# Performance work log

Measured on AMD Instinct MI355X. Metric: run time of the kernel, lower is better.

The kernel has to match this reference:

```python
import jax, jax.numpy as jnp
import numpy as np

EPS = 0.001  # additive floor applied after relu, as in the torch code


def setup_inputs() -> dict:
    key = jax.random.key(0)
    kA, kB, kW = jax.random.split(key, 3)
    M, N, C, H, W = 512, 64, 128, 8, 8
    A = jax.random.normal(kA, (M, C, H, W), dtype=jnp.float32)
    B = jax.random.normal(kB, (N, C, H, W), dtype=jnp.float32)
    Wg = jax.random.normal(kW, (C, C), dtype=jnp.float32) * 0.01  # Wg.data.normal_(0.0, 0.01)
    return {"A": A, "B": B, "Wg": Wg}


def reference(A, B, Wg):
    # Faithful vectorization of MIMOcom.get_source_dst_max(A, B, dir=True).
    # Torch loops i,j over HxW: B0 = B[:, i, j, :]; G = B0 @ Wg;
    # combination[m, n, p] = sum_c A[m, p, c] * G[n, c]; running max over (i, j).
    M, C, H, W = A.shape
    N = B.shape[0]
    P = H * W
    Af = jnp.transpose(A, (0, 2, 3, 1)).reshape(M, P, C)  # [M, P, C]
    Bf = jnp.transpose(B, (0, 2, 3, 1)).reshape(N, P, C)  # [N, Q, C]
    G = Bf @ Wg                                           # [N, Q, D]
    scores = jnp.einsum('mpd,nqd->mnpq', Af, G)           # [M, N, P, Q]
    comb_max = scores.max(axis=-1)                        # max over B positions q
    return jax.nn.relu(comb_max) + EPS                    # [M, N, P]
```

## Files before the change

### kernel.cpp

```cpp
#include <hip/hip_runtime.h>
#include <hip/hip_bf16.h>
#include <stdint.h>

typedef __attribute__((ext_vector_type(8))) short bf16x8;
typedef __attribute__((ext_vector_type(4))) float f32x4;
typedef __attribute__((ext_vector_type(16))) float f32x16;
using bf16 = __hip_bfloat16;

static constexpr int Mdim = 512;
static constexpr int Ndim = 64;
static constexpr int Cdim = 128;
static constexpr int Pdim = 64;
static constexpr float EPS_ADD = 0.001f;

#define SB0 __builtin_amdgcn_sched_barrier(0)
#define WAITV(N) asm volatile("s_waitcnt vmcnt(" #N ")" ::: "memory")

__device__ __forceinline__ void gll16(const void* gsrc, void* ldst) {
    const __attribute__((address_space(1))) unsigned int* g =
        (const __attribute__((address_space(1))) unsigned int*)gsrc;
    __attribute__((address_space(3))) unsigned int* l =
        (__attribute__((address_space(3))) unsigned int*)(uintptr_t)ldst;
    __builtin_amdgcn_global_load_lds(g, l, 16, 0, 0);
}

__global__ void prep_kernel(const float* __restrict__ A, const float* __restrict__ B,
                            const float* __restrict__ Wg,
                            bf16* __restrict__ Abf, bf16* __restrict__ Gbf) {
    __shared__ float lds[128 * 65];
    const int t = threadIdx.x;

    if (blockIdx.x < 512) {
        const int m = blockIdx.x;
        const float* __restrict__ Am = A + (size_t)m * (Cdim * Pdim);
#pragma unroll
        for (int i = 0; i < 8; ++i) {
            int v = t + i * 256;
            int gidx = v * 4;
            int c = gidx >> 6, p = gidx & 63;
            float4 val = *reinterpret_cast<const float4*>(Am + gidx);
            float* dst = &lds[c * 65 + p];
            dst[0] = val.x; dst[1] = val.y; dst[2] = val.z; dst[3] = val.w;
        }
        __syncthreads();

        bf16* __restrict__ dstm = Abf + (size_t)m * (Pdim * Cdim);
#pragma unroll
        for (int i = 0; i < 16; ++i) {
            int pr = t + i * 256;
            int p = pr >> 6;
            int c = (pr & 63) << 1;
            float f0 = lds[c * 65 + p];
            float f1 = lds[(c + 1) * 65 + p];
            union { bf16 h[2]; unsigned u; } pk;
            pk.h[0] = __float2bfloat16(f0);
            pk.h[1] = __float2bfloat16(f1);
            *reinterpret_cast<unsigned*>(dstm + p * Cdim + c) = pk.u;
        }
    } else {
        const int nb = blockIdx.x - 512;
        const int n  = nb >> 2;
        const int q0 = (nb & 3) * 16;
        const float* __restrict__ Bn = B + (size_t)n * (Cdim * Pdim);
#pragma unroll
        for (int i = 0; i < 8; ++i) {
            int v = t + i * 256;
            int gidx = v * 4;
            int c = gidx >> 6, q = gidx & 63;
            float4 val = *reinterpret_cast<const float4*>(Bn + gidx);
            float* dst = &lds[c * 65 + q];
            dst[0] = val.x; dst[1] = val.y; dst[2] = val.z; dst[3] = val.w;
        }
        __syncthreads();

        const int d  = t & 127;
        const int qb = q0 + (t >> 7) * 8;
        float acc[8] = {0.f, 0.f, 0.f, 0.f, 0.f, 0.f, 0.f, 0.f};
        for (int c = 0; c < 128; ++c) {
            float w = Wg[c * 128 + d];
#pragma unroll
            for (int qi = 0; qi < 8; ++qi)
                acc[qi] = fmaf(lds[c * 65 + qb + qi], w, acc[qi]);
        }
#pragma unroll
        for (int qi = 0; qi < 8; ++qi)
            Gbf[(size_t)(n * 64 + qb + qi) * Cdim + d] = __float2bfloat16(acc[qi]);
    }
}

__global__ __launch_bounds__(256, 2)
void gemm_max_kernel(const bf16* __restrict__ Abf, const bf16* __restrict__ Gbf,
                     float* __restrict__ out) {
    __shared__ bf16 sA[2][64 * 128];
    const int tid  = threadIdx.x;
    const int lane = tid & 63;
    const int w    = tid >> 6;
    const int nw = w >> 1, h = w & 1;
    const int l31 = lane & 31, hi = lane >> 5;
    const int mg = blockIdx.x & 31;
    const int bn = blockIdx.x >> 5;
    const int n  = bn * 2 + nw;

    const char* Abase = (const char*)Abf + (size_t)mg * 16 * 16384;
    auto stageA = [&](int s) {
        char* dst = (char*)&sA[s & 1][0];
        const char* src = Abase + (size_t)s * 16384;
#pragma unroll
        for (int i = 0; i < 4; ++i) {
            int f = (i * 256 + tid) * 16;
            int row = f >> 8;
            int inner = (f & 255) ^ ((row & 7) << 4);
            gll16(src + row * 256 + inner, dst + f);
        }
    };
    stageA(0);

    bf16x8 gf[2][8];
    {
        const bf16* Gp = Gbf + ((size_t)n * 64 + l31) * 128 + hi * 8;
#pragma unroll
        for (int qt = 0; qt < 2; ++qt)
#pragma unroll
            for (int ks = 0; ks < 8; ++ks)
                gf[qt][ks] = *reinterpret_cast<const bf16x8*>(Gp + qt * 32 * 128 + ks * 16);
    }

    f32x16 acc[2];
    const f32x16 z16 = {0.f,0.f,0.f,0.f,0.f,0.f,0.f,0.f,0.f,0.f,0.f,0.f,0.f,0.f,0.f,0.f};

    auto compute = [&](int s) {
        const char* ab = (const char*)&sA[s & 1][0] + (h * 32 + l31) * 256;
#pragma unroll
        for (int ks = 0; ks < 8; ++ks) {
            const int off = (ks * 32 + hi * 16) ^ ((l31 & 7) << 4);
            bf16x8 a = *reinterpret_cast<const bf16x8*>(ab + off);
            acc[0] = __builtin_amdgcn_mfma_f32_32x32x16_bf16(
                gf[0][ks], a, ks == 0 ? z16 : acc[0], 0, 0, 0);
            acc[1] = __builtin_amdgcn_mfma_f32_32x32x16_bf16(
                gf[1][ks], a, ks == 0 ? z16 : acc[1], 0, 0, 0);
        }
    };

    auto epilogue = [&](int s) {
        float v = acc[0][0];
#pragma unroll
        for (int j = 1; j < 16; ++j) v = fmaxf(v, acc[0][j]);
#pragma unroll
        for (int j = 0; j < 16; ++j) v = fmaxf(v, acc[1][j]);
        v = fmaxf(v, __shfl_xor(v, 32));
        if (hi == 0)
            out[(size_t)(mg * 16 + s) * 4096 + n * 64 + h * 32 + l31] =
                fmaxf(v, 0.f) + EPS_ADD;
    };

    WAITV(16); __builtin_amdgcn_s_barrier(); SB0;
    compute(0); SB0; stageA(1); epilogue(0); SB0;

    for (int s = 1; s <= 14; ++s) {
        WAITV(1); __builtin_amdgcn_s_barrier(); SB0;
        compute(s); SB0; stageA(s + 1); epilogue(s); SB0;
    }

    WAITV(1); __builtin_amdgcn_s_barrier(); SB0;
    compute(15); epilogue(15);
}

extern "C" void kernel_launch(void* const* d_in, const int* in_sizes, int n_in,
                              void* d_out, int out_size, void* d_ws, size_t ws_size,
                              hipStream_t stream) {
    const float* A  = (const float*)d_in[0];
    const float* B  = (const float*)d_in[1];
    const float* Wg = (const float*)d_in[2];
    float* out = (float*)d_out;

    bf16* Abf = (bf16*)d_ws;
    bf16* Gbf = (bf16*)((char*)d_ws + (size_t)Mdim * Pdim * Cdim * sizeof(bf16));

    prep_kernel<<<768, 256, 0, stream>>>(A, B, Wg, Abf, Gbf);
    gemm_max_kernel<<<1024, 256, 0, stream>>>(Abf, Gbf, out);
}
```

Baseline: 52.80 us.

## Pre-swizzle A and G into MFMA fragment layout and load A directly to registers

```diff
diff --git a/kernel.cpp b/kernel.cpp
--- a/kernel.cpp
+++ b/kernel.cpp
@@ -3,7 +3,6 @@
 #include <stdint.h>
 
 typedef __attribute__((ext_vector_type(8))) short bf16x8;
-typedef __attribute__((ext_vector_type(4))) float f32x4;
 typedef __attribute__((ext_vector_type(16))) float f32x16;
 using bf16 = __hip_bfloat16;
 
@@ -14,19 +13,10 @@
 static constexpr float EPS_ADD = 0.001f;
 
 #define SB0 __builtin_amdgcn_sched_barrier(0)
-#define WAITV(N) asm volatile("s_waitcnt vmcnt(" #N ")" ::: "memory")
-
-__device__ __forceinline__ void gll16(const void* gsrc, void* ldst) {
-    const __attribute__((address_space(1))) unsigned int* g =
-        (const __attribute__((address_space(1))) unsigned int*)gsrc;
-    __attribute__((address_space(3))) unsigned int* l =
-        (__attribute__((address_space(3))) unsigned int*)(uintptr_t)ldst;
-    __builtin_amdgcn_global_load_lds(g, l, 16, 0, 0);
-}
 
 __global__ void prep_kernel(const float* __restrict__ A, const float* __restrict__ B,
                             const float* __restrict__ Wg,
-                            bf16* __restrict__ Abf, bf16* __restrict__ Gbf) {
+                            bf16* __restrict__ Afrag, bf16* __restrict__ Gfrag) {
     __shared__ float lds[128 * 65];
     const int t = threadIdx.x;
 
@@ -44,7 +34,7 @@
         }
         __syncthreads();
 
-        bf16* __restrict__ dstm = Abf + (size_t)m * (Pdim * Cdim);
+        unsigned* __restrict__ dst32 = (unsigned*)(Afrag + (size_t)m * 8192);
 #pragma unroll
         for (int i = 0; i < 16; ++i) {
             int pr = t + i * 256;
@@ -52,10 +42,12 @@
             int c = (pr & 63) << 1;
             float f0 = lds[c * 65 + p];
             float f1 = lds[(c + 1) * 65 + p];
-            union { bf16 h[2]; unsigned u; } pk;
-            pk.h[0] = __float2bfloat16(f0);
-            pk.h[1] = __float2bfloat16(f1);
-            *reinterpret_cast<unsigned*>(dstm + p * Cdim + c) = pk.u;
+            union { bf16 hh[2]; unsigned u; } pk;
+            pk.hh[0] = __float2bfloat16(f0);
+            pk.hh[1] = __float2bfloat16(f1);
+            int h = p >> 5, l31 = p & 31;
+            int ks = c >> 4, hi = (c >> 3) & 1, e = c & 7;
+            dst32[h * 2048 + ks * 256 + hi * 128 + l31 * 4 + (e >> 1)] = pk.u;
         }
     } else {
         const int nb = blockIdx.x - 512;
@@ -82,16 +74,20 @@
             for (int qi = 0; qi < 8; ++qi)
                 acc[qi] = fmaf(lds[c * 65 + qb + qi], w, acc[qi]);
         }
+        bf16* __restrict__ gdst = Gfrag + (size_t)n * 8192;
+        const int ks = d >> 4, hi = (d >> 3) & 1, e = d & 7;
 #pragma unroll
-        for (int qi = 0; qi < 8; ++qi)
-            Gbf[(size_t)(n * 64 + qb + qi) * Cdim + d] = __float2bfloat16(acc[qi]);
+        for (int qi = 0; qi < 8; ++qi) {
+            int q = qb + qi;
+            int qt = q >> 5, l31 = q & 31;
+            gdst[qt * 4096 + ks * 512 + hi * 256 + l31 * 8 + e] = __float2bfloat16(acc[qi]);
+        }
     }
 }
 
 __global__ __launch_bounds__(256, 2)
-void gemm_max_kernel(const bf16* __restrict__ Abf, const bf16* __restrict__ Gbf,
+void gemm_max_kernel(const bf16* __restrict__ Afrag, const bf16* __restrict__ Gfrag,
                      float* __restrict__ out) {
-    __shared__ bf16 sA[2][64 * 128];
     const int tid  = threadIdx.x;
     const int lane = tid & 63;
     const int w    = tid >> 6;
@@ -100,69 +96,72 @@
     const int mg = blockIdx.x & 31;
     const int bn = blockIdx.x >> 5;
     const int n  = bn * 2 + nw;
-
-    const char* Abase = (const char*)Abf + (size_t)mg * 16 * 16384;
-    auto stageA = [&](int s) {
-        char* dst = (char*)&sA[s & 1][0];
-        const char* src = Abase + (size_t)s * 16384;
-#pragma unroll
-        for (int i = 0; i < 4; ++i) {
-            int f = (i * 256 + tid) * 16;
-            int row = f >> 8;
-            int inner = (f & 255) ^ ((row & 7) << 4);
-            gll16(src + row * 256 + inner, dst + f);
-        }
-    };
-    stageA(0);
+    const int phase = bn & 15;
 
     bf16x8 gf[2][8];
     {
-        const bf16* Gp = Gbf + ((size_t)n * 64 + l31) * 128 + hi * 8;
+        const bf16* Gp = Gfrag + (size_t)n * 8192 + lane * 8;
 #pragma unroll
         for (int qt = 0; qt < 2; ++qt)
 #pragma unroll
             for (int ks = 0; ks < 8; ++ks)
-                gf[qt][ks] = *reinterpret_cast<const bf16x8*>(Gp + qt * 32 * 128 + ks * 16);
+                gf[qt][ks] = *reinterpret_cast<const bf16x8*>(Gp + qt * 4096 + ks * 512);
     }
 
-    f32x16 acc[2];
+    const bf16* Ab = Afrag + (size_t)mg * 16 * 8192 + h * 4096 + lane * 8;
+    auto loadA = [&](bf16x8 (&dst)[8], int se) {
+        const bf16* p = Ab + (size_t)se * 8192;
+#pragma unroll
+        for (int ks = 0; ks < 8; ++ks)
+            dst[ks] = *reinterpret_cast<const bf16x8*>(p + ks * 512);
+    };
+
+    f32x16 acc0, acc1;
     const f32x16 z16 = {0.f,0.f,0.f,0.f,0.f,0.f,0.f,0.f,0.f,0.f,0.f,0.f,0.f,0.f,0.f,0.f};
 
-    auto compute = [&](int s) {
-        const char* ab = (const char*)&sA[s & 1][0] + (h * 32 + l31) * 256;
+    auto compute = [&](const bf16x8 (&a)[8]) {
 #pragma unroll
         for (int ks = 0; ks < 8; ++ks) {
-            const int off = (ks * 32 + hi * 16) ^ ((l31 & 7) << 4);
-            bf16x8 a = *reinterpret_cast<const bf16x8*>(ab + off);
-            acc[0] = __builtin_amdgcn_mfma_f32_32x32x16_bf16(
-                gf[0][ks], a, ks == 0 ? z16 : acc[0], 0, 0, 0);
-            acc[1] = __builtin_amdgcn_mfma_f32_32x32x16_bf16(
-                gf[1][ks], a, ks == 0 ? z16 : acc[1], 0, 0, 0);
+            acc0 = __builtin_amdgcn_mfma_f32_32x32x16_bf16(
+                gf[0][ks], a[ks], ks == 0 ? z16 : acc0, 0, 0, 0);
+            acc1 = __builtin_amdgcn_mfma_f32_32x32x16_bf16(
+                gf[1][ks], a[ks], ks == 0 ? z16 : acc1, 0, 0, 0);
         }
     };
 
-    auto epilogue = [&](int s) {
-        float v = acc[0][0];
+    auto epilogue = [&](int se) {
+        float v01 = fmaxf(acc0[0], acc0[1]);
 #pragma unroll
-        for (int j = 1; j < 16; ++j) v = fmaxf(v, acc[0][j]);
+        for (int j = 2; j < 16; ++j) v01 = fmaxf(v01, acc0[j]);
+        float v23 = fmaxf(acc1[0], acc1[1]);
 #pragma unroll
-        for (int j = 0; j < 16; ++j) v = fmaxf(v, acc[1][j]);
+        for (int j = 2; j < 16; ++j) v23 = fmaxf(v23, acc1[j]);
+        float v = fmaxf(v01, v23);
         v = fmaxf(v, __shfl_xor(v, 32));
         if (hi == 0)
-            out[(size_t)(mg * 16 + s) * 4096 + n * 64 + h * 32 + l31] =
+            out[(size_t)(mg * 16 + se) * 4096 + n * 64 + h * 32 + l31] =
                 fmaxf(v, 0.f) + EPS_ADD;
     };
 
-    WAITV(16); __builtin_amdgcn_s_barrier(); SB0;
-    compute(0); SB0; stageA(1); epilogue(0); SB0;
+    bf16x8 aA[8], aB[8];
+    loadA(aA, phase);
 
-    for (int s = 1; s <= 14; ++s) {
-        WAITV(1); __builtin_amdgcn_s_barrier(); SB0;
-        compute(s); SB0; stageA(s + 1); epilogue(s); SB0;
+#pragma unroll
+    for (int s = 0; s < 16; ++s) {
+        const int se = (s + phase) & 15;
+        const int sn = (s + 1 + phase) & 15;
+        if ((s & 1) == 0) {
+            if (s < 15) loadA(aB, sn);
+            SB0;
+            compute(aA);
+            epilogue(se);
+        } else {
+            if (s < 15) loadA(aA, sn);
+            SB0;
+            compute(aB);
+            epilogue(se);
+        }
     }
-
-    WAITV(1); __builtin_amdgcn_s_barrier(); SB0;
-    compute(15); epilogue(15);
 }
 
 extern "C" void kernel_launch(void* const* d_in, const int* in_sizes, int n_in,
@@ -173,9 +172,9 @@
     const float* Wg = (const float*)d_in[2];
     float* out = (float*)d_out;
 
-    bf16* Abf = (bf16*)d_ws;
-    bf16* Gbf = (bf16*)((char*)d_ws + (size_t)Mdim * Pdim * Cdim * sizeof(bf16));
+    bf16* Afrag = (bf16*)d_ws;
+    bf16* Gfrag = (bf16*)((char*)d_ws + (size_t)Mdim * Pdim * Cdim * sizeof(bf16));
 
-    prep_kernel<<<768, 256, 0, stream>>>(A, B, Wg, Abf, Gbf);
-    gemm_max_kernel<<<1024, 256, 0, stream>>>(Abf, Gbf, out);
+    prep_kernel<<<768, 256, 0, stream>>>(A, B, Wg, Afrag, Gfrag);
+    gemm_max_kernel<<<1024, 256, 0, stream>>>(Afrag, Gfrag, out);
 }
```

Result: slower. 55.83 us (+5.8%).
